# Kernel optimization log

Hardware: AMD Instinct MI355X
Metric: run time of the kernel (lower is better)

Reference implementation:

```python
import jax, jax.numpy as jnp
import numpy as np

B, L, DM = 4, 1024, 2048
H, KV, HD = 32, 4, 128
G = H // KV
E, TOPK, MI = 16, 8, 128
EPS = 1e-6
THETA = 1e6


def rms_norm(x, w):
    return x * jax.lax.rsqrt(jnp.mean(x * x, axis=-1, keepdims=True) + EPS) * w


def rotate_half(x):
    x1, x2 = jnp.split(x, 2, axis=-1)
    return jnp.concatenate([-x2, x1], axis=-1)


def setup_inputs() -> dict:
    key = jax.random.key(0)
    ks = jax.random.split(key, 10)
    s = 0.02
    # RoPE tables: [L, HD] broadcast to [B, L, HD]
    inv_freq = 1.0 / (THETA ** (jnp.arange(0, HD, 2, dtype=jnp.float32) / HD))
    ang = jnp.arange(L, dtype=jnp.float32)[:, None] * inv_freq[None, :]
    emb = jnp.concatenate([ang, ang], axis=-1)
    cos = jnp.broadcast_to(jnp.cos(emb)[None], (B, L, HD)).astype(jnp.float32)
    sin = jnp.broadcast_to(jnp.sin(emb)[None], (B, L, HD)).astype(jnp.float32)
    return {
        "x": jax.random.normal(ks[0], (B, L, DM), jnp.float32),
        "cos": cos,
        "sin": sin,
        "norm_attn_w": jnp.ones((DM,), jnp.float32),
        "q_w": jax.random.normal(ks[1], (H * HD, DM), jnp.float32) * s,
        "k_w": jax.random.normal(ks[2], (KV * HD, DM), jnp.float32) * s,
        "v_w": jax.random.normal(ks[3], (KV * HD, DM), jnp.float32) * s,
        "qn_w": jnp.ones((HD,), jnp.float32),
        "kn_w": jnp.ones((HD,), jnp.float32),
        "o_w": jax.random.normal(ks[4], (DM, H * HD), jnp.float32) * s,
        "norm_mlp_w": jnp.ones((DM,), jnp.float32),
        "router_w": jax.random.normal(ks[5], (E, DM), jnp.float32) * s,
        "egw": jax.random.normal(ks[6], (E, MI, DM), jnp.float32) * s,
        "euw": jax.random.normal(ks[7], (E, MI, DM), jnp.float32) * s,
        "edw": jax.random.normal(ks[8], (E, DM, MI), jnp.float32) * s,
    }


def _layer(x, cos, sin, norm_attn_w, q_w, k_w, v_w, qn_w, kn_w, o_w,
           norm_mlp_w, router_w, egw, euw, edw):
    b, l, dm = x.shape
    # ---- attention sub-block ----
    h = rms_norm(x, norm_attn_w)
    q = rms_norm((h @ q_w.T).reshape(b, l, H, HD), qn_w).swapaxes(1, 2)   # [B,H,L,D]
    k = rms_norm((h @ k_w.T).reshape(b, l, KV, HD), kn_w).swapaxes(1, 2)  # [B,KV,L,D]
    v = (h @ v_w.T).reshape(b, l, KV, HD).swapaxes(1, 2)                  # [B,KV,L,D]
    c = cos[:, None]  # [B,1,L,D]
    s = sin[:, None]
    q = c * q + s * rotate_half(q)
    k = c * k + s * rotate_half(k)
    # GQA: repeat kv heads
    k = jnp.repeat(k, G, axis=1)  # [B,H,L,D]
    v = jnp.repeat(v, G, axis=1)
    scores = jnp.einsum("bhqd,bhkd->bhqk", q, k) / jnp.sqrt(jnp.float32(HD))
    causal = jnp.tril(jnp.ones((l, l), bool))
    scores = jnp.where(causal[None, None], scores, jnp.float32(-1e30))
    attn = jax.nn.softmax(scores, axis=-1)
    o = jnp.einsum("bhqk,bhkd->bhqd", attn, v).swapaxes(1, 2).reshape(b, l, H * HD)
    x = x + o @ o_w.T
    # ---- sparse MoE MLP ----
    hm = rms_norm(x, norm_mlp_w).reshape(b * l, dm)  # [N,DM]
    logits = hm @ router_w.T                          # [N,E]
    probs = jax.nn.softmax(logits.astype(jnp.float32), axis=-1)
    rw, sel = jax.lax.top_k(probs, TOPK)              # [N,TOPK]
    rw = (rw / rw.sum(axis=-1, keepdims=True)).astype(x.dtype)
    n = b * l
    # dense combine weights [N,E] (topk indices are unique per token)
    w_dense = jnp.zeros((n, E), x.dtype).at[jnp.arange(n)[:, None], sel].add(rw)

    def body(acc, inp):
        gw, uw, dw, we = inp  # gw/uw [MI,DM], dw [DM,MI], we [N]
        a = jax.nn.silu(hm @ gw.T) * (hm @ uw.T)      # [N,MI]
        return acc + (a @ dw.T) * we[:, None], None

    out, _ = jax.lax.scan(body, jnp.zeros_like(hm), (egw, euw, edw, w_dense.T))
    return x + out.reshape(b, l, dm)


def reference(x, cos, sin, norm_attn_w, q_w, k_w, v_w, qn_w, kn_w, o_w,
              norm_mlp_w, router_w, egw, euw, edw):
    return _layer(x, cos, sin, norm_attn_w, q_w, k_w, v_w, qn_w, kn_w, o_w,
                  norm_mlp_w, router_w, egw, euw, edw)
```

## Files before the change

### kernel.cpp

```cpp
#include <hip/hip_runtime.h>
#include <stdint.h>

typedef _Float16 f16x8 __attribute__((ext_vector_type(8)));
typedef _Float16 f16x4 __attribute__((ext_vector_type(4)));
typedef float    f32x4 __attribute__((ext_vector_type(4)));

__device__ __forceinline__ void load16_lds(const _Float16* g, _Float16* l) {
    __builtin_amdgcn_global_load_lds(
        (const __attribute__((address_space(1))) void*)g,
        (__attribute__((address_space(3))) void*)l, 16, 0, 0);
}


__global__ void k_cast4(const float* __restrict__ q, const float* __restrict__ k,
                        const float* __restrict__ v, const float* __restrict__ o,
                        _Float16* __restrict__ qkvw, _Float16* __restrict__ ow)
{
    size_t i = ((size_t)blockIdx.x * 256 + threadIdx.x) * 4;
    const float* src; _Float16* dst;
    if (i < 8388608)        { src = q + i;            dst = qkvw + i; }
    else if (i < 9437184)   { src = k + (i - 8388608); dst = qkvw + i; }
    else if (i < 10485760)  { src = v + (i - 9437184); dst = qkvw + i; }
    else                    { src = o + (i - 10485760); dst = ow + (i - 10485760); }
    float4 x = *reinterpret_cast<const float4*>(src);
    f16x4 y = { (_Float16)x.x, (_Float16)x.y, (_Float16)x.z, (_Float16)x.w };
    *reinterpret_cast<f16x4*>(dst) = y;
}

__global__ void k_cast_dw(const float* __restrict__ edw, _Float16* __restrict__ dwc) {
    int t = blockIdx.x * 256 + threadIdx.x;
    int mi4 = (t & 31) * 4;
    int dm = (t >> 5) & 2047;
    int e = t >> 16;
    float4 v = *reinterpret_cast<const float4*>(edw + (((size_t)e * 2048 + dm) << 7) + mi4);
    f16x4 o = { (_Float16)v.x, (_Float16)v.y, (_Float16)v.z, (_Float16)v.w };
    *reinterpret_cast<f16x4*>(dwc + ((size_t)dm << 11) + e * 128 + mi4) = o;
}

__global__ __launch_bounds__(256) void k_cast_guw(
    const float* __restrict__ eg, const float* __restrict__ eu,
    _Float16* __restrict__ out)
{
    const int row = blockIdx.x;
    const int e = row >> 8, rem = row & 255, half = rem >> 7, mi = rem & 127;
    const float* src = (half ? eu : eg) + ((size_t)(e * 128 + mi)) * 2048;
    const int c = threadIdx.x * 8;
    float4 v0 = *reinterpret_cast<const float4*>(src + c);
    float4 v1 = *reinterpret_cast<const float4*>(src + c + 4);
    f16x8 o = { (_Float16)v0.x,(_Float16)v0.y,(_Float16)v0.z,(_Float16)v0.w,
                (_Float16)v1.x,(_Float16)v1.y,(_Float16)v1.z,(_Float16)v1.w };
    *reinterpret_cast<f16x8*>(out + (size_t)row * 2048 + c) = o;
}

__global__ __launch_bounds__(256) void k_rmsnorm(
    const float* __restrict__ x, const float* __restrict__ w,
    _Float16* __restrict__ oh)
{
    const int row = blockIdx.x, tid = threadIdx.x;
    const float* xr = x + (size_t)row * 2048;
    float4 a = *reinterpret_cast<const float4*>(xr + tid * 8);
    float4 b = *reinterpret_cast<const float4*>(xr + tid * 8 + 4);
    float ss = a.x*a.x + a.y*a.y + a.z*a.z + a.w*a.w
             + b.x*b.x + b.y*b.y + b.z*b.z + b.w*b.w;
    #pragma unroll
    for (int m = 1; m < 64; m <<= 1) ss += __shfl_xor(ss, m);
    __shared__ float red[4];
    if ((tid & 63) == 0) red[tid >> 6] = ss;
    __syncthreads();
    float tot = red[0] + red[1] + red[2] + red[3];
    float r = rsqrtf(tot * (1.f / 2048.f) + 1e-6f);
    float4 wa = *reinterpret_cast<const float4*>(w + tid * 8);
    float4 wb = *reinterpret_cast<const float4*>(w + tid * 8 + 4);
    f16x8 hv = { (_Float16)(a.x*r*wa.x), (_Float16)(a.y*r*wa.y),
                 (_Float16)(a.z*r*wa.z), (_Float16)(a.w*r*wa.w),
                 (_Float16)(b.x*r*wb.x), (_Float16)(b.y*r*wb.y),
                 (_Float16)(b.z*r*wb.z), (_Float16)(b.w*r*wb.w) };
    *reinterpret_cast<f16x8*>(oh + (size_t)row * 2048 + tid * 8) = hv;
}

__global__ __launch_bounds__(256) void k_gemm(
    const _Float16* __restrict__ A, int lda,
    const _Float16* __restrict__ W, int ldw,
    float* __restrict__ Cf, _Float16* __restrict__ Ch, int ldc,
    const float* __restrict__ resid, int K)
{
    __shared__ __align__(16) _Float16 As[3][128][32];
    __shared__ __align__(16) _Float16 Ws[3][128][32];
    const int r0 = blockIdx.x * 128, c0 = blockIdx.y * 128;
    const int tid = threadIdx.x, lane = tid & 63, wid = tid >> 6;
    const int wr = wid >> 1, wc = wid & 1;
    const int sr = lane >> 2;
    const int scs = ((lane & 3) ^ ((lane >> 3) & 3)) * 8;
    const int fr = lane & 15;
    const int rks = (((lane >> 4) ^ ((fr >> 1) & 3))) * 8;
    const f32x4 z4 = { 0.f, 0.f, 0.f, 0.f };
    f32x4 acc[4][4];
    #pragma unroll
    for (int i = 0; i < 4; i++)
        #pragma unroll
        for (int j = 0; j < 4; j++) acc[i][j] = z4;

    auto stage = [&](int bf, int k0) {
        #pragma unroll
        for (int i = 0; i < 2; i++) {
            int ch = wid * 2 + i;
            load16_lds(A + (size_t)(r0 + ch * 16 + sr) * lda + k0 + scs, &As[bf][ch * 16][0]);
            load16_lds(W + (size_t)(c0 + ch * 16 + sr) * ldw + k0 + scs, &Ws[bf][ch * 16][0]);
        }
    };

    const int nt = K >> 5;
    stage(0, 0);
    if (nt > 1) stage(1, 32);
    int cur = 0;
    for (int t = 0; t < nt; t++) {
        if (t < nt - 1) asm volatile("s_waitcnt vmcnt(4)" ::: "memory");
        else            asm volatile("s_waitcnt vmcnt(0)" ::: "memory");
        __builtin_amdgcn_s_barrier();
        f16x8 af[4], bf4[4];
        #pragma unroll
        for (int i = 0; i < 4; i++)
            af[i] = *reinterpret_cast<const f16x8*>(&As[cur][wr * 64 + i * 16 + fr][rks]);
        #pragma unroll
        for (int j = 0; j < 4; j++)
            bf4[j] = *reinterpret_cast<const f16x8*>(&Ws[cur][wc * 64 + j * 16 + fr][rks]);
        if (t + 2 < nt) stage((t + 2) % 3, (t + 2) << 5);
        __builtin_amdgcn_s_setprio(1);
        #pragma unroll
        for (int i = 0; i < 4; i++)
            #pragma unroll
            for (int j = 0; j < 4; j++)
                acc[i][j] = __builtin_amdgcn_mfma_f32_16x16x32_f16(af[i], bf4[j], acc[i][j], 0, 0, 0);
        __builtin_amdgcn_s_setprio(0);
        cur = (cur + 1) % 3;
    }
    #pragma unroll
    for (int i = 0; i < 4; i++) {
        const int rowb = r0 + wr * 64 + i * 16 + (lane >> 4) * 4;
        #pragma unroll
        for (int j = 0; j < 4; j++) {
            const int col = c0 + wc * 64 + j * 16 + fr;
            #pragma unroll
            for (int r = 0; r < 4; r++) {
                size_t idx = (size_t)(rowb + r) * ldc + col;
                float v = acc[i][j][r];
                if (resid) v += resid[idx];
                if (Ch) Ch[idx] = (_Float16)v;
                else    Cf[idx] = v;
            }
        }
    }
}

__global__ __launch_bounds__(512, 2) void k_gemm8(
    const _Float16* __restrict__ A, int lda,
    const _Float16* __restrict__ W, int ldw,
    _Float16* __restrict__ Ch, int ldc, int K)
{
    __shared__ __align__(16) _Float16 As[3][256][32];
    __shared__ __align__(16) _Float16 Ws[3][256][32];
    const int r0 = blockIdx.x * 256, c0 = blockIdx.y * 256;
    const int tid = threadIdx.x, lane = tid & 63, wid = tid >> 6;
    const int wr = wid >> 2, wc = wid & 3;
    const int rA = lane >> 2;
    const int scs = ((lane & 3) ^ ((lane >> 3) & 3)) * 8;
    const int fr = lane & 15;
    const int rks = (((lane >> 4) ^ ((fr >> 1) & 3))) * 8;
    const f32x4 z4 = { 0.f, 0.f, 0.f, 0.f };
    f32x4 acc[8][4];
    #pragma unroll
    for (int i = 0; i < 8; i++)
        #pragma unroll
        for (int j = 0; j < 4; j++) acc[i][j] = z4;

    auto stage = [&](int bf, int k0) {
        #pragma unroll
        for (int i = 0; i < 2; i++) {
            load16_lds(A + (size_t)(r0 + i * 128 + wid * 16 + rA) * lda + k0 + scs,
                       &As[bf][i * 128 + wid * 16][0]);
            load16_lds(W + (size_t)(c0 + i * 128 + wid * 16 + rA) * ldw + k0 + scs,
                       &Ws[bf][i * 128 + wid * 16][0]);
        }
    };

    const int nt = K >> 5;
    stage(0, 0);
    if (nt > 1) stage(1, 32);
    int cur = 0;
    for (int t = 0; t < nt; t++) {
        if (t < nt - 1) asm volatile("s_waitcnt vmcnt(4)" ::: "memory");
        else            asm volatile("s_waitcnt vmcnt(0)" ::: "memory");
        __builtin_amdgcn_s_barrier();
        f16x8 af[8], bf4[4];
        #pragma unroll
        for (int i = 0; i < 8; i++)
            af[i] = *reinterpret_cast<const f16x8*>(&As[cur][wr * 128 + i * 16 + fr][rks]);
        #pragma unroll
        for (int j = 0; j < 4; j++)
            bf4[j] = *reinterpret_cast<const f16x8*>(&Ws[cur][wc * 64 + j * 16 + fr][rks]);
        if (t + 2 < nt) stage((t + 2) % 3, (t + 2) << 5);
        __builtin_amdgcn_s_setprio(1);
        #pragma unroll
        for (int i = 0; i < 8; i++)
            #pragma unroll
            for (int j = 0; j < 4; j++)
                acc[i][j] = __builtin_amdgcn_mfma_f32_16x16x32_f16(af[i], bf4[j], acc[i][j], 0, 0, 0);
        __builtin_amdgcn_s_setprio(0);
        cur = (cur + 1) % 3;
    }
    #pragma unroll
    for (int i = 0; i < 8; i++) {
        const int rowb = r0 + wr * 128 + i * 16 + (lane >> 4) * 4;
        #pragma unroll
        for (int j = 0; j < 4; j++) {
            const int col = c0 + wc * 64 + j * 16 + fr;
            #pragma unroll
            for (int r = 0; r < 4; r++)
                Ch[(size_t)(rowb + r) * ldc + col] = (_Float16)acc[i][j][r];
        }
    }
}

__global__ __launch_bounds__(256) void k_gu_comb(
    const _Float16* __restrict__ gucat, const float* __restrict__ wdense,
    _Float16* __restrict__ ab)
{
    const int tok = blockIdx.x;
    const int idx = threadIdx.x;
    const int e = idx >> 4, mi8 = (idx & 15) * 8;
    const _Float16* gp = gucat + (size_t)tok * 4096 + e * 256 + mi8;
    f16x8 gv = *reinterpret_cast<const f16x8*>(gp);
    f16x8 uv = *reinterpret_cast<const f16x8*>(gp + 128);
    float wv = wdense[(size_t)e * 4096 + tok];
    f16x8 o;
    #pragma unroll
    for (int j = 0; j < 8; j++) {
        float g = (float)gv[j], u = (float)uv[j];
        float sil = g / (1.f + __expf(-g));
        o[j] = (_Float16)(sil * u * wv);
    }
    *reinterpret_cast<f16x8*>(ab + (size_t)tok * 2048 + e * 128 + mi8) = o;
}

__global__ __launch_bounds__(256) void k_qkv_post(
    const _Float16* __restrict__ qkv,
    const float* __restrict__ cosb, const float* __restrict__ sinb,
    const float* __restrict__ qn_w, const float* __restrict__ kn_w,
    _Float16* __restrict__ qh, _Float16* __restrict__ kh)
{
    const int tok = blockIdx.x;
    const int u = blockIdx.y * 4 + (threadIdx.x >> 6);
    const int lane = threadIdx.x & 63;
    const int b = tok >> 10, l = tok & 1023;
    const float c0 = cosb[(size_t)tok * 128 + lane];
    const float c1 = cosb[(size_t)tok * 128 + lane + 64];
    const float s0 = sinb[(size_t)tok * 128 + lane];
    const float s1 = sinb[(size_t)tok * 128 + lane + 64];
    if (u < 32) {
        const _Float16* base = qkv + (size_t)tok * 5120 + u * 128;
        float v0 = (float)base[lane], v1 = (float)base[lane + 64];
        float ss = v0 * v0 + v1 * v1;
        #pragma unroll
        for (int m = 1; m < 64; m <<= 1) ss += __shfl_xor(ss, m);
        float rms = rsqrtf(ss * (1.f / 128.f) + 1e-6f);
        float n0 = v0 * rms * qn_w[lane], n1 = v1 * rms * qn_w[lane + 64];
        _Float16* o = qh + (size_t)tok * 4096 + u * 128;
        o[lane]      = (_Float16)(c0 * n0 - s0 * n1);
        o[lane + 64] = (_Float16)(c1 * n1 + s1 * n0);
    } else {
        const int kvh = u - 32;
        const _Float16* base = qkv + (size_t)tok * 5120 + 4096 + kvh * 128;
        float v0 = (float)base[lane], v1 = (float)base[lane + 64];
        float ss = v0 * v0 + v1 * v1;
        #pragma unroll
        for (int m = 1; m < 64; m <<= 1) ss += __shfl_xor(ss, m);
        float rms = rsqrtf(ss * (1.f / 128.f) + 1e-6f);
        float n0 = v0 * rms * kn_w[lane], n1 = v1 * rms * kn_w[lane + 64];
        _Float16* o = kh + (((size_t)(b * 4 + kvh)) * 1024 + l) * 128;
        o[lane]      = (_Float16)(c0 * n0 - s0 * n1);
        o[lane + 64] = (_Float16)(c1 * n1 + s1 * n0);
    }
}

__global__ __launch_bounds__(256) void k_vt(
    const _Float16* __restrict__ qkv, _Float16* __restrict__ vth)
{
    const int bkv = blockIdx.x;
    const int b = bkv >> 2, kv = bkv & 3;
    const int l0 = blockIdx.y * 64, d0 = blockIdx.z * 64;
    __shared__ _Float16 T[64][72];
    const int t = threadIdx.x;
    const int r = t >> 3, c8 = (t & 7) * 8;
    #pragma unroll
    for (int rr = 0; rr < 2; rr++) {
        int l = l0 + r + rr * 32;
        *reinterpret_cast<f16x8*>(&T[r + rr * 32][c8]) =
            *reinterpret_cast<const f16x8*>(
                qkv + (size_t)(b * 1024 + l) * 5120 + 4608 + kv * 128 + d0 + c8);
    }
    __syncthreads();
    #pragma unroll
    for (int rr = 0; rr < 2; rr++) {
        int d = d0 + r + rr * 32;
        f16x8 v;
        #pragma unroll
        for (int j = 0; j < 8; j++) v[j] = T[c8 + j][r + rr * 32];
        *reinterpret_cast<f16x8*>(vth + ((size_t)(bkv * 128 + d)) * 1024 + l0 + c8) = v;
    }
}

__global__ __launch_bounds__(256) void k_attn(
    const _Float16* __restrict__ qh, const _Float16* __restrict__ kh,
    const _Float16* __restrict__ vth, _Float16* __restrict__ oh)
{
    const int bh = blockIdx.x;
    const int g = 15 - blockIdx.y;
    const int b = bh >> 5, h = bh & 31, kv = h >> 3;
    const int tid = threadIdx.x, lane = tid & 63, wid = tid >> 6;
    const int fr = lane & 15, fg = lane >> 4;
    const int q0w = g * 64 + wid * 16;

    __shared__ __align__(16) _Float16 Ks[64][128];
    __shared__ __align__(16) _Float16 Vs[128][64];
    __shared__ __align__(16) _Float16 Ps[4][16][72];

    const _Float16* kb = kh + ((size_t)(b * 4 + kv)) * 1024 * 128;
    const _Float16* vb = vth + ((size_t)(b * 4 + kv)) * 128 * 1024;

    f16x8 aq[4];
    {
        const _Float16* qbase = qh + ((size_t)(b * 1024 + q0w + fr)) * 4096 + h * 128;
        #pragma unroll
        for (int kk = 0; kk < 4; kk++)
            aq[kk] = *reinterpret_cast<const f16x8*>(qbase + kk * 32 + fg * 8);
    }

    float m_r[4] = { -1e30f, -1e30f, -1e30f, -1e30f };
    float l_r[4] = { 0.f, 0.f, 0.f, 0.f };
    const f32x4 z4 = { 0.f, 0.f, 0.f, 0.f };
    f32x4 oacc[8];
    #pragma unroll
    for (int dj = 0; dj < 8; dj++) oacc[dj] = z4;

    const int ntiles = g + 1;
    for (int kt = 0; kt < ntiles; kt++) {
        const int key0 = kt * 64;
        #pragma unroll
        for (int i = 0; i < 4; i++) {
            int rr = 16 * wid + 4 * i + (lane >> 4);
            int c16 = (lane & 15) ^ (rr & 7);
            load16_lds(kb + (size_t)(key0 + rr) * 128 + c16 * 8,
                       &Ks[0][0] + (16 * wid + 4 * i) * 128);
        }
        #pragma unroll
        for (int i = 0; i < 4; i++) {
            int rr = 32 * wid + 8 * i + (lane >> 3);
            int c16 = (lane & 7) ^ (rr & 7);
            load16_lds(vb + (size_t)rr * 1024 + key0 + c16 * 8,
                       &Vs[0][0] + (32 * wid + 8 * i) * 64);
        }
        __syncthreads();

        f32x4 sc[4];
        #pragma unroll
        for (int j = 0; j < 4; j++) sc[j] = z4;
        #pragma unroll
        for (int j = 0; j < 4; j++) {
            #pragma unroll
            for (int kk = 0; kk < 4; kk++) {
                f16x8 bk = *reinterpret_cast<const f16x8*>(
                    &Ks[0][0] + (j * 16 + fr) * 128 + (((kk * 4 + fg) ^ (fr & 7)) * 8));
                sc[j] = __builtin_amdgcn_mfma_f32_16x16x32_f16(aq[kk], bk, sc[j], 0, 0, 0);
            }
        }

        const bool lastt = (kt == ntiles - 1);
        float pmax[4] = { -1e30f, -1e30f, -1e30f, -1e30f };
        #pragma unroll
        for (int j = 0; j < 4; j++) {
            const int key = key0 + j * 16 + fr;
            #pragma unroll
            for (int r = 0; r < 4; r++) {
                float v = sc[j][r] * 0.08838834764831845f;
                if (lastt && key > q0w + fg * 4 + r) v = -1e30f;
                sc[j][r] = v;
                pmax[r] = fmaxf(pmax[r], v);
            }
        }
        #pragma unroll
        for (int m = 1; m < 16; m <<= 1)
            #pragma unroll
            for (int r = 0; r < 4; r++) pmax[r] = fmaxf(pmax[r], __shfl_xor(pmax[r], m));
        float alpha[4];
        #pragma unroll
        for (int r = 0; r < 4; r++) {
            float mn = fmaxf(m_r[r], pmax[r]);
            alpha[r] = __expf(m_r[r] - mn);
            m_r[r] = mn;
        }
        float rs[4] = { 0.f, 0.f, 0.f, 0.f };
        #pragma unroll
        for (int j = 0; j < 4; j++)
            #pragma unroll
            for (int r = 0; r < 4; r++) {
                float p = __expf(sc[j][r] - m_r[r]);
                sc[j][r] = p;
                rs[r] += p;
            }
        #pragma unroll
        for (int m = 1; m < 16; m <<= 1)
            #pragma unroll
            for (int r = 0; r < 4; r++) rs[r] += __shfl_xor(rs[r], m);
        #pragma unroll
        for (int r = 0; r < 4; r++) l_r[r] = l_r[r] * alpha[r] + rs[r];
        #pragma unroll
        for (int dj = 0; dj < 8; dj++)
            #pragma unroll
            for (int r = 0; r < 4; r++) oacc[dj][r] *= alpha[r];

        #pragma unroll
        for (int j = 0; j < 4; j++)
            #pragma unroll
            for (int r = 0; r < 4; r++)
                Ps[wid][fg * 4 + r][j * 16 + fr] = (_Float16)sc[j][r];

        #pragma unroll
        for (int ks = 0; ks < 2; ks++) {
            f16x8 ap = *reinterpret_cast<const f16x8*>(&Ps[wid][fr][ks * 32 + fg * 8]);
            #pragma unroll
            for (int dj = 0; dj < 8; dj++) {
                f16x8 bv = *reinterpret_cast<const f16x8*>(
                    &Vs[0][0] + (dj * 16 + fr) * 64 + (((ks * 4 + fg) ^ (fr & 7)) * 8));
                oacc[dj] = __builtin_amdgcn_mfma_f32_16x16x32_f16(ap, bv, oacc[dj], 0, 0, 0);
            }
        }
        __syncthreads();
    }

    float inv[4];
    #pragma unroll
    for (int r = 0; r < 4; r++) inv[r] = 1.f / l_r[r];
    #pragma unroll
    for (int dj = 0; dj < 8; dj++)
        #pragma unroll
        for (int r = 0; r < 4; r++)
            oh[((size_t)(b * 1024 + q0w + fg * 4 + r)) * 4096 + h * 128 + dj * 16 + fr] =
                (_Float16)(oacc[dj][r] * inv[r]);
}

__global__ __launch_bounds__(256) void k_router(
    const float* __restrict__ x2, const float* __restrict__ wm,
    const float* __restrict__ rw, float* __restrict__ wdense)
{
    const int tok = blockIdx.x * 4 + (threadIdx.x >> 6);
    const int lane = threadIdx.x & 63;
    __shared__ float lg[4][16];
    const float* hr = x2 + (size_t)tok * 2048;
    float vals[32];
    float ss = 0.f;
    #pragma unroll
    for (int i = 0; i < 32; i++) { float v = hr[i * 64 + lane]; vals[i] = v; ss += v * v; }
    #pragma unroll
    for (int m = 1; m < 64; m <<= 1) ss += __shfl_xor(ss, m);
    float r = rsqrtf(ss * (1.f / 2048.f) + 1e-6f);
    #pragma unroll
    for (int i = 0; i < 32; i++) vals[i] *= r * wm[i * 64 + lane];
    for (int e = 0; e < 16; e++) {
        float acc = 0.f;
        #pragma unroll
        for (int i = 0; i < 32; i++) acc += vals[i] * rw[(size_t)e * 2048 + i * 64 + lane];
        #pragma unroll
        for (int m = 1; m < 64; m <<= 1) acc += __shfl_xor(acc, m);
        if (lane == 0) lg[threadIdx.x >> 6][e] = acc;
    }
    __syncthreads();
    if (lane == 0) {
        float* l = lg[threadIdx.x >> 6];
        float mx = l[0];
        for (int e = 1; e < 16; e++) mx = fmaxf(mx, l[e]);
        float p[16]; float sum = 0.f;
        for (int e = 0; e < 16; e++) { p[e] = expf(l[e] - mx); sum += p[e]; }
        for (int e = 0; e < 16; e++) p[e] /= sum;
        bool sel[16]; for (int e = 0; e < 16; e++) sel[e] = false;
        float ssum = 0.f;
        for (int t = 0; t < 8; t++) {
            int bi = -1; float bv = -1.f;
            for (int e = 0; e < 16; e++) if (!sel[e] && p[e] > bv) { bv = p[e]; bi = e; }
            sel[bi] = true; ssum += bv;
        }
        for (int e = 0; e < 16; e++)
            wdense[(size_t)e * 4096 + tok] = sel[e] ? p[e] / ssum : 0.f;
    }
}


extern "C" void kernel_launch(void* const* d_in, const int* in_sizes, int n_in,
                              void* d_out, int out_size, void* d_ws, size_t ws_size,
                              hipStream_t stream)
{
    const float* x        = (const float*)d_in[0];
    const float* cosb     = (const float*)d_in[1];
    const float* sinb     = (const float*)d_in[2];
    const float* nattn    = (const float*)d_in[3];
    const float* q_w      = (const float*)d_in[4];
    const float* k_w      = (const float*)d_in[5];
    const float* v_w      = (const float*)d_in[6];
    const float* qn_w     = (const float*)d_in[7];
    const float* kn_w     = (const float*)d_in[8];
    const float* o_w      = (const float*)d_in[9];
    const float* nmlp     = (const float*)d_in[10];
    const float* router_w = (const float*)d_in[11];
    const float* egw      = (const float*)d_in[12];
    const float* euw      = (const float*)d_in[13];
    const float* edw      = (const float*)d_in[14];

    char* w = (char*)d_ws;
    _Float16* qkvw_h = (_Float16*)(w + 0);
    _Float16* ow_h   = (_Float16*)(w + 20971520);
    _Float16* guw_h  = (_Float16*)(w + 37748736);
    _Float16* dwc_h  = (_Float16*)(w + 54525952);
    _Float16* h_h    = (_Float16*)(w + 62914560);
    _Float16* hm_h   = h_h;
    float*    x2     = (float*)(w + 79691776);
    _Float16* qkv_h  = (_Float16*)(w + 113246208);
    _Float16* o_h    = qkv_h;
    _Float16* ab_h   = qkv_h;
    _Float16* q_h    = (_Float16*)(w + 155189248);
    _Float16* gucat  = (_Float16*)(w + 155189248);
    _Float16* k_h    = (_Float16*)(w + 188743680);
    _Float16* vt_h   = (_Float16*)(w + 192937984);
    float*    wdense = (float*)(w + 197132288);

    k_cast4<<<18432, 256, 0, stream>>>(q_w, k_w, v_w, o_w, qkvw_h, ow_h);
    k_cast_guw<<<4096, 256, 0, stream>>>(egw, euw, guw_h);
    k_cast_dw<<<4096, 256, 0, stream>>>(edw, dwc_h);

    k_rmsnorm<<<4096, 256, 0, stream>>>(x, nattn, h_h);
    k_gemm8<<<dim3(16, 16), 512, 0, stream>>>(h_h, 2048, qkvw_h, 2048, qkv_h, 5120, 2048);
    k_gemm<<<dim3(32, 8), 256, 0, stream>>>(h_h, 2048, qkvw_h + (size_t)4096 * 2048, 2048,
                                            nullptr, qkv_h + 4096, 5120, nullptr, 2048);
    k_qkv_post<<<dim3(4096, 9), 256, 0, stream>>>(qkv_h, cosb, sinb, qn_w, kn_w, q_h, k_h);
    k_vt<<<dim3(16, 16, 2), 256, 0, stream>>>(qkv_h, vt_h);
    k_attn<<<dim3(128, 16), 256, 0, stream>>>(q_h, k_h, vt_h, o_h);
    k_gemm<<<dim3(32, 16), 256, 0, stream>>>(o_h, 4096, ow_h, 4096,
                                             x2, nullptr, 2048, x, 4096);
    k_rmsnorm<<<4096, 256, 0, stream>>>(x2, nmlp, hm_h);
    k_router<<<1024, 256, 0, stream>>>(x2, nmlp, router_w, wdense);
    k_gemm8<<<dim3(16, 16), 512, 0, stream>>>(hm_h, 2048, guw_h, 2048, gucat, 4096, 2048);
    k_gu_comb<<<4096, 256, 0, stream>>>(gucat, wdense, ab_h);
    k_gemm<<<dim3(32, 16), 256, 0, stream>>>(ab_h, 2048, dwc_h, 2048,
                                             (float*)d_out, nullptr, 2048, x2, 2048);

    (void)in_sizes; (void)n_in; (void)out_size; (void)ws_size;
}
```

Baseline: 528.4 us.

## Restructure attention softmax: fold scale into Q, exp2, lazy rescale, MFMA row-sum

```diff
diff --git a/kernel.cpp b/kernel.cpp
--- a/kernel.cpp
+++ b/kernel.cpp
@@ -50,6 +50,13 @@
     f16x8 o = { (_Float16)v0.x,(_Float16)v0.y,(_Float16)v0.z,(_Float16)v0.w,
                 (_Float16)v1.x,(_Float16)v1.y,(_Float16)v1.z,(_Float16)v1.w };
     *reinterpret_cast<f16x8*>(out + (size_t)row * 2048 + c) = o;
+}
+
+__global__ void k_ones(_Float16* __restrict__ p) {
+    int i = blockIdx.x * 256 + threadIdx.x;
+    _Float16 v = (i < 256) ? (_Float16)1.0f : (_Float16)0.0f;
+    f16x4 o = { v, v, v, v };
+    *reinterpret_cast<f16x4*>(p + i * 4) = o;
 }
 
 __global__ __launch_bounds__(256) void k_rmsnorm(
@@ -252,6 +259,7 @@
     const int u = blockIdx.y * 4 + (threadIdx.x >> 6);
     const int lane = threadIdx.x & 63;
     const int b = tok >> 10, l = tok & 1023;
+    const float SCL = 0.12752887074166638f;
     const float c0 = cosb[(size_t)tok * 128 + lane];
     const float c1 = cosb[(size_t)tok * 128 + lane + 64];
     const float s0 = sinb[(size_t)tok * 128 + lane];
@@ -265,8 +273,8 @@
         float rms = rsqrtf(ss * (1.f / 128.f) + 1e-6f);
         float n0 = v0 * rms * qn_w[lane], n1 = v1 * rms * qn_w[lane + 64];
         _Float16* o = qh + (size_t)tok * 4096 + u * 128;
-        o[lane]      = (_Float16)(c0 * n0 - s0 * n1);
-        o[lane + 64] = (_Float16)(c1 * n1 + s1 * n0);
+        o[lane]      = (_Float16)(SCL * (c0 * n0 - s0 * n1));
+        o[lane + 64] = (_Float16)(SCL * (c1 * n1 + s1 * n0));
     } else {
         const int kvh = u - 32;
         const _Float16* base = qkv + (size_t)tok * 5120 + 4096 + kvh * 128;
@@ -311,7 +319,8 @@
 
 __global__ __launch_bounds__(256) void k_attn(
     const _Float16* __restrict__ qh, const _Float16* __restrict__ kh,
-    const _Float16* __restrict__ vth, _Float16* __restrict__ oh)
+    const _Float16* __restrict__ vth, const _Float16* __restrict__ ones16,
+    _Float16* __restrict__ oh)
 {
     const int bh = blockIdx.x;
     const int g = 15 - blockIdx.y;
@@ -321,7 +330,7 @@
     const int q0w = g * 64 + wid * 16;
 
     __shared__ __align__(16) _Float16 Ks[64][128];
-    __shared__ __align__(16) _Float16 Vs[128][64];
+    __shared__ __align__(16) _Float16 Vs[144][64];
     __shared__ __align__(16) _Float16 Ps[4][16][72];
 
     const _Float16* kb = kh + ((size_t)(b * 4 + kv)) * 1024 * 128;
@@ -336,11 +345,10 @@
     }
 
     float m_r[4] = { -1e30f, -1e30f, -1e30f, -1e30f };
-    float l_r[4] = { 0.f, 0.f, 0.f, 0.f };
     const f32x4 z4 = { 0.f, 0.f, 0.f, 0.f };
-    f32x4 oacc[8];
-    #pragma unroll
-    for (int dj = 0; dj < 8; dj++) oacc[dj] = z4;
+    f32x4 oacc[9];
+    #pragma unroll
+    for (int dj = 0; dj < 9; dj++) oacc[dj] = z4;
 
     const int ntiles = g + 1;
     for (int kt = 0; kt < ntiles; kt++) {
@@ -348,7 +356,7 @@
         #pragma unroll
         for (int i = 0; i < 4; i++) {
             int rr = 16 * wid + 4 * i + (lane >> 4);
-            int c16 = (lane & 15) ^ (rr & 7);
+            int c16 = (lane & 15) ^ (rr & 15);
             load16_lds(kb + (size_t)(key0 + rr) * 128 + c16 * 8,
                        &Ks[0][0] + (16 * wid + 4 * i) * 128);
         }
@@ -359,6 +367,12 @@
             load16_lds(vb + (size_t)rr * 1024 + key0 + c16 * 8,
                        &Vs[0][0] + (32 * wid + 8 * i) * 64);
         }
+        if (wid < 2) {
+            int rr = wid * 8 + (lane >> 3);
+            int c16 = (lane & 7) ^ (rr & 7);
+            load16_lds(ones16 + (size_t)rr * 1024 + key0 + c16 * 8,
+                       &Vs[0][0] + (128 + wid * 8) * 64);
+        }
         __syncthreads();
 
         f32x4 sc[4];
@@ -369,7 +383,7 @@
             #pragma unroll
             for (int kk = 0; kk < 4; kk++) {
                 f16x8 bk = *reinterpret_cast<const f16x8*>(
-                    &Ks[0][0] + (j * 16 + fr) * 128 + (((kk * 4 + fg) ^ (fr & 7)) * 8));
+                    &Ks[0][0] + (j * 16 + fr) * 128 + (((kk * 4 + fg) ^ fr) * 8));
                 sc[j] = __builtin_amdgcn_mfma_f32_16x16x32_f16(aq[kk], bk, sc[j], 0, 0, 0);
             }
         }
@@ -381,7 +395,7 @@
             const int key = key0 + j * 16 + fr;
             #pragma unroll
             for (int r = 0; r < 4; r++) {
-                float v = sc[j][r] * 0.08838834764831845f;
+                float v = sc[j][r];
                 if (lastt && key > q0w + fg * 4 + r) v = -1e30f;
                 sc[j][r] = v;
                 pmax[r] = fmaxf(pmax[r], v);
@@ -391,32 +405,24 @@
         for (int m = 1; m < 16; m <<= 1)
             #pragma unroll
             for (int r = 0; r < 4; r++) pmax[r] = fmaxf(pmax[r], __shfl_xor(pmax[r], m));
-        float alpha[4];
-        #pragma unroll
-        for (int r = 0; r < 4; r++) {
-            float mn = fmaxf(m_r[r], pmax[r]);
-            alpha[r] = __expf(m_r[r] - mn);
-            m_r[r] = mn;
-        }
-        float rs[4] = { 0.f, 0.f, 0.f, 0.f };
+
+        float dm = fmaxf(fmaxf(pmax[0] - m_r[0], pmax[1] - m_r[1]),
+                         fmaxf(pmax[2] - m_r[2], pmax[3] - m_r[3]));
+        if (__any(dm > 8.f)) {
+            #pragma unroll
+            for (int r = 0; r < 4; r++) {
+                float mn = fmaxf(m_r[r], pmax[r]);
+                float alpha = __builtin_amdgcn_exp2f(m_r[r] - mn);
+                m_r[r] = mn;
+                #pragma unroll
+                for (int dj = 0; dj < 9; dj++) oacc[dj][r] *= alpha;
+            }
+        }
         #pragma unroll
         for (int j = 0; j < 4; j++)
             #pragma unroll
-            for (int r = 0; r < 4; r++) {
-                float p = __expf(sc[j][r] - m_r[r]);
-                sc[j][r] = p;
-                rs[r] += p;
-            }
-        #pragma unroll
-        for (int m = 1; m < 16; m <<= 1)
-            #pragma unroll
-            for (int r = 0; r < 4; r++) rs[r] += __shfl_xor(rs[r], m);
-        #pragma unroll
-        for (int r = 0; r < 4; r++) l_r[r] = l_r[r] * alpha[r] + rs[r];
-        #pragma unroll
-        for (int dj = 0; dj < 8; dj++)
-            #pragma unroll
-            for (int r = 0; r < 4; r++) oacc[dj][r] *= alpha[r];
+            for (int r = 0; r < 4; r++)
+                sc[j][r] = __builtin_amdgcn_exp2f(sc[j][r] - m_r[r]);
 
         #pragma unroll
         for (int j = 0; j < 4; j++)
@@ -428,7 +434,7 @@
         for (int ks = 0; ks < 2; ks++) {
             f16x8 ap = *reinterpret_cast<const f16x8*>(&Ps[wid][fr][ks * 32 + fg * 8]);
             #pragma unroll
-            for (int dj = 0; dj < 8; dj++) {
+            for (int dj = 0; dj < 9; dj++) {
                 f16x8 bv = *reinterpret_cast<const f16x8*>(
                     &Vs[0][0] + (dj * 16 + fr) * 64 + (((ks * 4 + fg) ^ (fr & 7)) * 8));
                 oacc[dj] = __builtin_amdgcn_mfma_f32_16x16x32_f16(ap, bv, oacc[dj], 0, 0, 0);
@@ -439,7 +445,10 @@
 
     float inv[4];
     #pragma unroll
-    for (int r = 0; r < 4; r++) inv[r] = 1.f / l_r[r];
+    for (int r = 0; r < 4; r++) {
+        float l = __shfl(oacc[8][r], lane & 48);
+        inv[r] = 1.f / l;
+    }
     #pragma unroll
     for (int dj = 0; dj < 8; dj++)
         #pragma unroll
@@ -530,10 +539,12 @@
     _Float16* k_h    = (_Float16*)(w + 188743680);
     _Float16* vt_h   = (_Float16*)(w + 192937984);
     float*    wdense = (float*)(w + 197132288);
+    _Float16* ones_h = (_Float16*)(w + 197394432);
 
     k_cast4<<<18432, 256, 0, stream>>>(q_w, k_w, v_w, o_w, qkvw_h, ow_h);
     k_cast_guw<<<4096, 256, 0, stream>>>(egw, euw, guw_h);
     k_cast_dw<<<4096, 256, 0, stream>>>(edw, dwc_h);
+    k_ones<<<16, 256, 0, stream>>>(ones_h);
 
     k_rmsnorm<<<4096, 256, 0, stream>>>(x, nattn, h_h);
     k_gemm8<<<dim3(16, 16), 512, 0, stream>>>(h_h, 2048, qkvw_h, 2048, qkv_h, 5120, 2048);
@@ -541,7 +552,7 @@
                                             nullptr, qkv_h + 4096, 5120, nullptr, 2048);
     k_qkv_post<<<dim3(4096, 9), 256, 0, stream>>>(qkv_h, cosb, sinb, qn_w, kn_w, q_h, k_h);
     k_vt<<<dim3(16, 16, 2), 256, 0, stream>>>(qkv_h, vt_h);
-    k_attn<<<dim3(128, 16), 256, 0, stream>>>(q_h, k_h, vt_h, o_h);
+    k_attn<<<dim3(128, 16), 256, 0, stream>>>(q_h, k_h, vt_h, ones_h, o_h);
     k_gemm<<<dim3(32, 16), 256, 0, stream>>>(o_h, 4096, ow_h, 4096,
                                              x2, nullptr, 2048, x, 4096);
     k_rmsnorm<<<4096, 256, 0, stream>>>(x2, nmlp, hm_h);
```

Result: faster. 512.6 us (-3.0%).
